# Kernel tuning notes

Hardware: AMD Instinct MI355X
Metric: run time of the kernel (lower is better)

Reference implementation:

```python
import jax, jax.numpy as jnp
import numpy as np

N_NODES = 50000
N_EDGES = 1600000
D_FEAT = 128
EMB = 32
HEADS = 4
SLOPE = 0.2  # PyG GATv2 default negative_slope


def setup_inputs() -> dict:
    key = jax.random.key(0)
    ks = jax.random.split(key, 12)
    H, C = HEADS, EMB
    hid = H * C  # concat output dim = 128

    def glorot(k, shape):
        fan_in, fan_out = shape[0], shape[-1] if len(shape) > 1 else shape[0]
        lim = jnp.sqrt(6.0 / (fan_in + fan_out)).astype(jnp.float32)
        return jax.random.uniform(k, shape, jnp.float32, -lim, lim)

    x = jax.random.normal(ks[0], (N_NODES, D_FEAT), jnp.float32)
    edge_index = jax.random.randint(ks[1], (2, N_EDGES), 0, N_NODES, jnp.int32).astype(jnp.int64)

    return {
        "x": x,
        "edge_index": edge_index,
        # layer 1: in D_FEAT -> H*C (separate source/target lins, share_weights=False)
        "W1_l": glorot(ks[2], (D_FEAT, hid)),
        "W1_r": glorot(ks[3], (D_FEAT, hid)),
        "att1": glorot(ks[4], (H, C)),
        "b1": jnp.zeros((hid,), jnp.float32),
        # layer 2: in H*C -> H*C
        "W2_l": glorot(ks[5], (hid, hid)),
        "W2_r": glorot(ks[6], (hid, hid)),
        "att2": glorot(ks[7], (H, C)),
        "b2": jnp.zeros((hid,), jnp.float32),
    }


def _gatv2_layer(x, src, dst, W_l, W_r, att, bias, n_nodes):
    H, C = att.shape
    xl = (x @ W_l).reshape(n_nodes, H, C)  # source-side transform
    xr = (x @ W_r).reshape(n_nodes, H, C)  # target-side transform
    # per-edge pre-activation: GATv2 applies LeakyReLU BEFORE the attention dot
    msg = xl[src] + xr[dst]                               # [E, H, C]
    e = jnp.einsum('ehc,hc->eh', jax.nn.leaky_relu(msg, SLOPE), att)  # [E, H]
    # numerically stable segment softmax over incoming edges of each dst node
    m = jax.ops.segment_max(e, dst, num_segments=n_nodes)  # [N, H]
    ex = jnp.exp(e - m[dst])
    denom = jax.ops.segment_sum(ex, dst, num_segments=n_nodes)  # [N, H]
    alpha = ex / (denom[dst] + 1e-16)                     # [E, H]
    out = jax.ops.segment_sum(alpha[:, :, None] * xl[src], dst, num_segments=n_nodes)
    return out.reshape(n_nodes, H * C) + bias


def reference(x, edge_index, W1_l, W1_r, att1, b1, W2_l, W2_r, att2, b2):
    n = x.shape[0]
    # PyG default add_self_loops=True: append (i -> i) for every node
    loop = jnp.arange(n, dtype=edge_index.dtype)
    src = jnp.concatenate([edge_index[0], loop])
    dst = jnp.concatenate([edge_index[1], loop])
    h = jax.nn.relu(_gatv2_layer(x, src, dst, W1_l, W1_r, att1, b1, n))
    h = jax.nn.relu(_gatv2_layer(h, src, dst, W2_l, W2_r, att2, b2, n))
    return h
```

## Files before the change

### kernel.cpp

```cpp
#include <hip/hip_runtime.h>

#define N_NODES 50000
#define N_EDGES 1600000
#define ET (N_EDGES + N_NODES)
#define DF 128
#define SLOPE 0.2f

#define NB 196
#define BCAP 10240
#define P1_CHUNK 4096
#define GEMM_BLOCKS ((N_NODES + 63) / 64)
#define BIN_BLOCKS ((ET + P1_CHUNK - 1) / P1_CHUNK)

typedef __attribute__((ext_vector_type(4))) float floatx4;
typedef __attribute__((ext_vector_type(8))) _Float16 half8;
typedef __attribute__((ext_vector_type(2))) _Float16 half2v;

__global__ __launch_bounds__(256) void wconv4(
    const float* __restrict__ W0, const float* __restrict__ W1,
    const float* __restrict__ W2, const float* __restrict__ W3,
    _Float16* __restrict__ Wh, _Float16* __restrict__ Wl,
    int* __restrict__ g_count)
{
    if (blockIdx.x == 0) g_count[threadIdx.x] = 0;
    int idx = blockIdx.x * 256 + threadIdx.x;
    int m = idx >> 14, rem = idx & 16383;
    const float* W = (m == 0) ? W0 : (m == 1) ? W1 : (m == 2) ? W2 : W3;
    int c = rem >> 7, k = rem & 127;
    float v = W[k * 128 + c];
    _Float16 h = (_Float16)v;
    int slab = k >> 5, q = (k >> 3) & 3, j = k & 7;
    size_t o = (size_t)m * 16384 + (size_t)((slab << 2) + q) * 1024 + (c << 3) + j;
    Wh[o] = h;
    Wl[o] = (_Float16)(v - (float)h);
}

__device__ __forceinline__ half8 load_h8(const float* p) {
    float4 a = *(const float4*)(p);
    float4 b = *(const float4*)(p + 4);
    half8 h;
    h[0] = (_Float16)a.x; h[1] = (_Float16)a.y;
    h[2] = (_Float16)a.z; h[3] = (_Float16)a.w;
    h[4] = (_Float16)b.x; h[5] = (_Float16)b.y;
    h[6] = (_Float16)b.z; h[7] = (_Float16)b.w;
    return h;
}
__device__ __forceinline__ half8 load_h8(const _Float16* p) {
    return *(const half8*)p;
}

template<typename T>
__device__ __forceinline__ void gemm_body(
    int bid, const T* __restrict__ X,
    const _Float16* __restrict__ WhL, const _Float16* __restrict__ WlL,
    const _Float16* __restrict__ WhR, const _Float16* __restrict__ WlR,
    _Float16* __restrict__ outL, _Float16* __restrict__ outR, int M, char* smem_)
{
    _Float16* xs  = (_Float16*)smem_;
    _Float16* whL = xs + 64 * 40;
    _Float16* wlL = whL + 4096;
    _Float16* whR = wlL + 4096;
    _Float16* wlR = whR + 4096;

    const int t = threadIdx.x;
    const int row0 = bid * 64;
    const int lane = t & 63, wv = t >> 6;
    const int lm = lane & 15, quad = lane >> 4;
    const int m0 = wv * 16;

    floatx4 accL[8], accR[8];
#pragma unroll
    for (int i = 0; i < 8; i++) { accL[i] = (floatx4)0.f; accR[i] = (floatx4)0.f; }

    const int sr = t >> 2;
    const int sc = (t & 3) * 8;

    for (int kb = 0; kb < 128; kb += 32) {
        const int slab = kb >> 5;
        int xrow = row0 + sr; if (xrow >= M) xrow = M - 1;
        half8 xv = load_h8(X + (size_t)xrow * DF + kb + sc);
        *(half8*)&xs[sr * 40 + sc] = xv;

        {
            const size_t sbase = (size_t)slab * 4096;
            const _Float16* gsrc[4] = { WhL + sbase, WlL + sbase,
                                        WhR + sbase, WlR + sbase };
            _Float16* ldst[4] = { whL, wlL, whR, wlR };
#pragma unroll
            for (int b = 0; b < 4; b++) {
#pragma unroll
                for (int i = 0; i < 2; i++) {
                    const int chunk = wv * 2 + i;
                    const _Float16* src = gsrc[b] + chunk * 512 + lane * 8;
                    __builtin_amdgcn_global_load_lds(
                        (const __attribute__((address_space(1))) void*)src,
                        (__attribute__((address_space(3))) void*)(ldst[b] + chunk * 512),
                        16, 0, 0);
                }
            }
        }
        __syncthreads();

        half8 af = *(const half8*)&xs[(m0 + lm) * 40 + quad * 8];
#pragma unroll
        for (int nt = 0; nt < 8; nt++) {
            const int bofs = quad * 1024 + (nt * 16 + lm) * 8;
            half8 bh = *(const half8*)&whL[bofs];
            half8 bl = *(const half8*)&wlL[bofs];
            accL[nt] = __builtin_amdgcn_mfma_f32_16x16x32_f16(af, bh, accL[nt], 0, 0, 0);
            accL[nt] = __builtin_amdgcn_mfma_f32_16x16x32_f16(af, bl, accL[nt], 0, 0, 0);
            half8 ch = *(const half8*)&whR[bofs];
            half8 cl = *(const half8*)&wlR[bofs];
            accR[nt] = __builtin_amdgcn_mfma_f32_16x16x32_f16(af, ch, accR[nt], 0, 0, 0);
            accR[nt] = __builtin_amdgcn_mfma_f32_16x16x32_f16(af, cl, accR[nt], 0, 0, 0);
        }
        __syncthreads();
    }

#pragma unroll
    for (int nt = 0; nt < 8; nt++) {
        int col = (nt >> 2) * 64 + (nt & 3) * 16 + lm;
#pragma unroll
        for (int r = 0; r < 4; r++) {
            int gr = row0 + m0 + quad * 4 + r;
            if (gr < M) {
                size_t o = (size_t)gr * DF + col;
                outL[o] = (_Float16)accL[nt][r];
                outR[o] = (_Float16)accR[nt][r];
            }
        }
    }
}

__device__ __forceinline__ void bin_body(
    int bid, const int* __restrict__ ei,
    int* __restrict__ g_count, int* __restrict__ bucket_mem, char* smem_)
{
    int* cnt  = (int*)smem_;
    int* base = cnt + NB;
    int* cnt2 = base + NB;
    const int tid = threadIdx.x;

    for (int i = tid; i < NB; i += 256) { cnt[i] = 0; cnt2[i] = 0; }
    __syncthreads();

    const int e0 = bid * P1_CHUNK;
    int srcv[16], dstv[16];
#pragma unroll
    for (int i = 0; i < 16; i++) {
        int eid = e0 + i * 256 + tid;
        int s = 0, d = -1;
        if (eid < ET) {
            if (eid < N_EDGES) { s = ei[eid]; d = ei[N_EDGES + eid]; }
            else               { s = d = eid - N_EDGES; }
        }
        srcv[i] = s; dstv[i] = d;
        if (d >= 0) atomicAdd(&cnt[d >> 8], 1);
    }
    __syncthreads();
    for (int i = tid; i < NB; i += 256)
        base[i] = (cnt[i] > 0) ? atomicAdd(&g_count[i], cnt[i]) : 0;
    __syncthreads();
#pragma unroll
    for (int i = 0; i < 16; i++) {
        int d = dstv[i];
        if (d >= 0) {
            int b = d >> 8;
            int r = atomicAdd(&cnt2[b], 1);
            int slot = base[b] + r;
            if (slot < BCAP)
                bucket_mem[(size_t)b * BCAP + slot] =
                    (srcv[i] & 0xFFFF) | ((d & 255) << 16);
        }
    }
}

__global__ __launch_bounds__(256) void gemm_bin(
    const float* __restrict__ X,
    const _Float16* __restrict__ Wh, const _Float16* __restrict__ Wl,
    _Float16* __restrict__ outL, _Float16* __restrict__ outR,
    const int* __restrict__ ei,
    int* __restrict__ g_count, int* __restrict__ bucket_mem)
{
    __shared__ char smem[37888];
    if (blockIdx.x < GEMM_BLOCKS)
        gemm_body<float>(blockIdx.x, X, Wh, Wl, Wh + 16384, Wl + 16384,
                         outL, outR, N_NODES, smem);
    else
        bin_body(blockIdx.x - GEMM_BLOCKS, ei, g_count, bucket_mem, smem);
}

__global__ __launch_bounds__(256) void gemm_f16(
    const _Float16* __restrict__ X,
    const _Float16* __restrict__ Wh, const _Float16* __restrict__ Wl,
    _Float16* __restrict__ outL, _Float16* __restrict__ outR)
{
    __shared__ char smem[37888];
    gemm_body<_Float16>(blockIdx.x, X, Wh, Wl, Wh + 16384, Wl + 16384,
                        outL, outR, N_NODES, smem);
}

__global__ __launch_bounds__(1024) void csr_pass(const int* __restrict__ g_count,
                                                 const int* __restrict__ bucket_mem,
                                                 int* __restrict__ row_ptr,
                                                 unsigned short* __restrict__ csr_src)
{
    __shared__ int sh_edges[BCAP];
    __shared__ int hist[256], offs[256], excl[256], cnt2[256];
    __shared__ int gsc[256];
    const int b = blockIdx.x, tid = threadIdx.x;

    if (tid < 256) gsc[tid] = (tid < NB) ? g_count[tid] : 0;
    __syncthreads();
    for (int d = 1; d < 256; d <<= 1) {
        int x = 0;
        if (tid < 256 && tid >= d) x = gsc[tid - d];
        __syncthreads();
        if (tid < 256) gsc[tid] += x;
        __syncthreads();
    }
    const int base_csr = (b > 0) ? gsc[b - 1] : 0;

    int m = g_count[b]; if (m > BCAP) m = BCAP;
    if (tid < 256) { hist[tid] = 0; cnt2[tid] = 0; }
    __syncthreads();
    const int* bm = bucket_mem + (size_t)b * BCAP;
    for (int i = tid; i < m; i += 1024) {
        int p = bm[i];
        sh_edges[i] = p;
        atomicAdd(&hist[(p >> 16) & 255], 1);
    }
    __syncthreads();
    if (tid < 256) offs[tid] = hist[tid];
    __syncthreads();
    for (int d = 1; d < 256; d <<= 1) {
        int x = 0;
        if (tid < 256 && tid >= d) x = offs[tid - d];
        __syncthreads();
        if (tid < 256) offs[tid] += x;
        __syncthreads();
    }
    if (tid < 256) {
        excl[tid] = offs[tid] - hist[tid];
        int node = (b << 8) + tid;
        if (node < N_NODES) row_ptr[node] = base_csr + excl[tid];
    }
    if (b == 0 && tid == 0) row_ptr[N_NODES] = ET;
    __syncthreads();
    for (int i = tid; i < m; i += 1024) {
        int p = sh_edges[i];
        int dl = (p >> 16) & 255;
        int r = atomicAdd(&cnt2[dl], 1);
        csr_src[base_csr + excl[dl] + r] = (unsigned short)(p & 0xFFFF);
    }
}

template<typename TOut>
__global__ __launch_bounds__(256) void fused_agg(
    const _Float16* __restrict__ XL, const _Float16* __restrict__ XR,
    const int* __restrict__ row_ptr, const unsigned short* __restrict__ csr_src,
    const float* __restrict__ att, const float* __restrict__ bias,
    TOut* __restrict__ out)
{
    const int t = threadIdx.x;
    const int wave = t >> 6, l = t & 63;
    const int g = l >> 4, gl = l & 15;
    const int n = blockIdx.x * 4 + wave;
    if (n >= N_NODES) return;
    const int beg = row_ptr[n], end = row_ptr[n + 1];
    const int deg = end - beg;
    const int dlim = (deg < 128) ? deg : 128;

    const int liA = beg + l, liB = liA + 64;
    unsigned sa = (liA < end) ? (unsigned)csr_src[liA] : 0u;
    unsigned sb = (liB < end) ? (unsigned)csr_src[liB] : 0u;
    const unsigned s32 = sa | (sb << 16);

    const int c0 = gl * 8;
    half8 xrh = *(const half8*)(XR + (size_t)n * DF + c0);
    float4 at0 = *(const float4*)(att + c0);
    float4 at1 = *(const float4*)(att + c0 + 4);
    half2v a01 = { (_Float16)at0.x, (_Float16)at0.y };
    half2v a23 = { (_Float16)at0.z, (_Float16)at0.w };
    half2v a45 = { (_Float16)at1.x, (_Float16)at1.y };
    half2v a67 = { (_Float16)at1.z, (_Float16)at1.w };
    const half8 slp = { (_Float16)SLOPE, (_Float16)SLOPE, (_Float16)SLOPE, (_Float16)SLOPE,
                        (_Float16)SLOPE, (_Float16)SLOPE, (_Float16)SLOPE, (_Float16)SLOPE };

    float a0 = 0.f, a1 = 0.f, a2 = 0.f, a3 = 0.f;
    float a4 = 0.f, a5 = 0.f, a6 = 0.f, a7 = 0.f, den = 0.f;

#define SRC(POS)                                                               \
    ({ int _p = (POS);                                                         \
       unsigned _v = (unsigned)__shfl((int)s32, _p & 63);                      \
       (int)(((_p & 64) ? (_v >> 16) : _v) & 0xFFFFu); })
#define LDROW(S) (*(const half8*)(XL + ((size_t)(unsigned)(S) << 7) + c0))

#define EDGE_STEP(HV, EOK)                                                     \
    {                                                                          \
        const bool _ok = (EOK);                                                \
        half8 _msg = HV + xrh;                                                 \
        half8 _lk  = __builtin_elementwise_max(_msg, _msg * slp);              \
        half2v _m01 = { _lk[0], _lk[1] };                                      \
        half2v _m23 = { _lk[2], _lk[3] };                                      \
        half2v _m45 = { _lk[4], _lk[5] };                                      \
        half2v _m67 = { _lk[6], _lk[7] };                                      \
        float _sc = __builtin_amdgcn_fdot2(_m01, a01, 0.f, false);             \
        _sc = __builtin_amdgcn_fdot2(_m23, a23, _sc, false);                   \
        _sc = __builtin_amdgcn_fdot2(_m45, a45, _sc, false);                   \
        _sc = __builtin_amdgcn_fdot2(_m67, a67, _sc, false);                   \
        _sc += __shfl_xor(_sc, 1);                                             \
        _sc += __shfl_xor(_sc, 2);                                             \
        float _e = _ok ? __expf(_sc) : 0.f;                                    \
        uint4 _hw; __builtin_memcpy(&_hw, &(HV), 16);                          \
        asm("v_fma_mix_f32 %0, %1, %2, %0 op_sel:[0,0,0] op_sel_hi:[1,0,0]"    \
            : "+v"(a0) : "v"(_hw.x), "v"(_e));                                 \
        asm("v_fma_mix_f32 %0, %1, %2, %0 op_sel:[1,0,0] op_sel_hi:[1,0,0]"    \
            : "+v"(a1) : "v"(_hw.x), "v"(_e));                                 \
        asm("v_fma_mix_f32 %0, %1, %2, %0 op_sel:[0,0,0] op_sel_hi:[1,0,0]"    \
            : "+v"(a2) : "v"(_hw.y), "v"(_e));                                 \
        asm("v_fma_mix_f32 %0, %1, %2, %0 op_sel:[1,0,0] op_sel_hi:[1,0,0]"    \
            : "+v"(a3) : "v"(_hw.y), "v"(_e));                                 \
        asm("v_fma_mix_f32 %0, %1, %2, %0 op_sel:[0,0,0] op_sel_hi:[1,0,0]"    \
            : "+v"(a4) : "v"(_hw.z), "v"(_e));                                 \
        asm("v_fma_mix_f32 %0, %1, %2, %0 op_sel:[1,0,0] op_sel_hi:[1,0,0]"    \
            : "+v"(a5) : "v"(_hw.z), "v"(_e));                                 \
        asm("v_fma_mix_f32 %0, %1, %2, %0 op_sel:[0,0,0] op_sel_hi:[1,0,0]"    \
            : "+v"(a6) : "v"(_hw.w), "v"(_e));                                 \
        asm("v_fma_mix_f32 %0, %1, %2, %0 op_sel:[1,0,0] op_sel_hi:[1,0,0]"    \
            : "+v"(a7) : "v"(_hw.w), "v"(_e));                                 \
        den += _e;                                                             \
    }

    half8 X0 = LDROW(SRC(g));
    half8 X1 = LDROW(SRC(4 + g));
    half8 Y0 = LDROW(SRC(8 + g));
    half8 Y1 = LDROW(SRC(12 + g));

    int p = 0;
    for (;;) {
        EDGE_STEP(X0, (p + g < dlim))
        EDGE_STEP(X1, (p + 4 + g < dlim))
        X0 = LDROW(SRC(p + 16 + g));
        X1 = LDROW(SRC(p + 20 + g));
        p += 8;
        if (p >= dlim) break;
        EDGE_STEP(Y0, (p + g < dlim))
        EDGE_STEP(Y1, (p + 4 + g < dlim))
        Y0 = LDROW(SRC(p + 16 + g));
        Y1 = LDROW(SRC(p + 20 + g));
        p += 8;
        if (p >= dlim) break;
    }

    for (int q = 128; q < deg; q += 4) {
        int ei_ = beg + q + g;
        int s = (ei_ < end) ? (int)csr_src[ei_] : 0;
        half8 hvt = LDROW(s);
        EDGE_STEP(hvt, (q + g < deg))
    }
#undef EDGE_STEP
#undef SRC
#undef LDROW

#define CMB(x) x += __shfl_xor(x, 16); x += __shfl_xor(x, 32);
    CMB(a0) CMB(a1) CMB(a2) CMB(a3) CMB(a4) CMB(a5) CMB(a6) CMB(a7) CMB(den)
#undef CMB

    if (g == 0) {
        float inv = 1.f / (den + 1e-16f);
        float4 b0 = *(const float4*)(bias + c0);
        float4 b1 = *(const float4*)(bias + c0 + 4);
        float o[8];
        o[0] = fmaxf(a0 * inv + b0.x, 0.f);
        o[1] = fmaxf(a1 * inv + b0.y, 0.f);
        o[2] = fmaxf(a2 * inv + b0.z, 0.f);
        o[3] = fmaxf(a3 * inv + b0.w, 0.f);
        o[4] = fmaxf(a4 * inv + b1.x, 0.f);
        o[5] = fmaxf(a5 * inv + b1.y, 0.f);
        o[6] = fmaxf(a6 * inv + b1.z, 0.f);
        o[7] = fmaxf(a7 * inv + b1.w, 0.f);
        TOut* op = out + (size_t)n * DF + c0;
        if constexpr (sizeof(TOut) == 2) {
            half8 hv;
#pragma unroll
            for (int i = 0; i < 8; i++) hv[i] = (_Float16)o[i];
            *(half8*)op = hv;
        } else {
            *(float4*)(op)     = make_float4(o[0], o[1], o[2], o[3]);
            *(float4*)(op + 4) = make_float4(o[4], o[5], o[6], o[7]);
        }
    }
}

extern "C" void kernel_launch(void* const* d_in, const int* in_sizes, int n_in,
                              void* d_out, int out_size, void* d_ws, size_t ws_size,
                              hipStream_t stream)
{
    (void)in_sizes; (void)n_in; (void)out_size; (void)ws_size;

    const float* x    = (const float*)d_in[0];
    const int*   ei   = (const int*)d_in[1];
    const float* W1l  = (const float*)d_in[2];
    const float* W1r  = (const float*)d_in[3];
    const float* att1 = (const float*)d_in[4];
    const float* b1   = (const float*)d_in[5];
    const float* W2l  = (const float*)d_in[6];
    const float* W2r  = (const float*)d_in[7];
    const float* att2 = (const float*)d_in[8];
    const float* b2   = (const float*)d_in[9];
    float* out = (float*)d_out;

    char* ws = (char*)d_ws;
    size_t off = 0;
    const size_t NF = (size_t)N_NODES * DF * sizeof(float);
    _Float16* A = (_Float16*)(ws + off); off += NF / 2;
    _Float16* B = (_Float16*)(ws + off); off += NF / 2;
    _Float16* C = (_Float16*)(ws + off); off += NF / 2;
    int* bucket_mem  = (int*)(ws + off); off += (size_t)NB * BCAP * sizeof(int);
    int* g_count     = (int*)(ws + off); off += 256 * sizeof(int);
    int* row_ptr     = (int*)(ws + off); off += (size_t)(N_NODES + 1) * sizeof(int);
    unsigned short* csr_src = (unsigned short*)(ws + off);
    off += ((size_t)ET * sizeof(unsigned short) + 255) & ~(size_t)255;
    _Float16* Wh = (_Float16*)(ws + off); off += 4 * 16384 * sizeof(_Float16);
    _Float16* Wl = (_Float16*)(ws + off); off += 4 * 16384 * sizeof(_Float16);

    wconv4<<<256, 256, 0, stream>>>(W1l, W1r, W2l, W2r, Wh, Wl, g_count);

    gemm_bin<<<GEMM_BLOCKS + BIN_BLOCKS, 256, 0, stream>>>(
        x, Wh, Wl, A, B, ei, g_count, bucket_mem);
    csr_pass<<<NB, 1024, 0, stream>>>(g_count, bucket_mem, row_ptr, csr_src);
    fused_agg<_Float16><<<(N_NODES + 3) / 4, 256, 0, stream>>>(
        A, B, row_ptr, csr_src, att1, b1, C);

    gemm_f16<<<GEMM_BLOCKS, 256, 0, stream>>>(C, Wh + 2 * 16384, Wl + 2 * 16384, A, B);
    fused_agg<float><<<(N_NODES + 3) / 4, 256, 0, stream>>>(
        A, B, row_ptr, csr_src, att2, b2, out);
}
```

Baseline: 264.3 us.

## Regroup prep kernels: fuse weight conversion with binning, CSR build with GEMM

Edge binning moves out of the GEMM launch and into a new launch alongside weight conversion. The CSR build then runs as extra blocks beside the first-layer GEMM, which removes the standalone 1024-thread csr_pass launch. Buckets shrink from 256 to 128 destination nodes (391 buckets, capacity 6144) so each CSR block fits in 256 threads and shares the GEMM's shared-memory size. The g_count reset becomes a memset. The cost is one more launch (the memset), and bucket overflow is now silently dropped at a smaller per-bucket capacity.

```diff
diff --git a/kernel.cpp b/kernel.cpp
--- a/kernel.cpp
+++ b/kernel.cpp
@@ -6,24 +6,24 @@
 #define DF 128
 #define SLOPE 0.2f
 
-#define NB 196
-#define BCAP 10240
+#define NB2 391
+#define CAP2 6144
 #define P1_CHUNK 4096
 #define GEMM_BLOCKS ((N_NODES + 63) / 64)
 #define BIN_BLOCKS ((ET + P1_CHUNK - 1) / P1_CHUNK)
+#define WCONV_BLOCKS 256
 
 typedef __attribute__((ext_vector_type(4))) float floatx4;
 typedef __attribute__((ext_vector_type(8))) _Float16 half8;
 typedef __attribute__((ext_vector_type(2))) _Float16 half2v;
 
-__global__ __launch_bounds__(256) void wconv4(
+__device__ __forceinline__ void wconv_body(
+    int bid,
     const float* __restrict__ W0, const float* __restrict__ W1,
     const float* __restrict__ W2, const float* __restrict__ W3,
-    _Float16* __restrict__ Wh, _Float16* __restrict__ Wl,
-    int* __restrict__ g_count)
-{
-    if (blockIdx.x == 0) g_count[threadIdx.x] = 0;
-    int idx = blockIdx.x * 256 + threadIdx.x;
+    _Float16* __restrict__ Wh, _Float16* __restrict__ Wl)
+{
+    int idx = bid * 256 + threadIdx.x;
     int m = idx >> 14, rem = idx & 16383;
     const float* W = (m == 0) ? W0 : (m == 1) ? W1 : (m == 2) ? W2 : W3;
     int c = rem >> 7, k = rem & 127;
@@ -33,6 +33,63 @@
     size_t o = (size_t)m * 16384 + (size_t)((slab << 2) + q) * 1024 + (c << 3) + j;
     Wh[o] = h;
     Wl[o] = (_Float16)(v - (float)h);
+}
+
+__device__ __forceinline__ void bin_body(
+    int bid, const int* __restrict__ ei,
+    int* __restrict__ g_count, int* __restrict__ bucket_mem, char* smem_)
+{
+    int* cnt  = (int*)smem_;
+    int* base = cnt + NB2;
+    int* cnt2 = base + NB2;
+    const int tid = threadIdx.x;
+
+    for (int i = tid; i < NB2; i += 256) { cnt[i] = 0; cnt2[i] = 0; }
+    __syncthreads();
+
+    const int e0 = bid * P1_CHUNK;
+    int srcv[16], dstv[16];
+#pragma unroll
+    for (int i = 0; i < 16; i++) {
+        int eid = e0 + i * 256 + tid;
+        int s = 0, d = -1;
+        if (eid < ET) {
+            if (eid < N_EDGES) { s = ei[eid]; d = ei[N_EDGES + eid]; }
+            else               { s = d = eid - N_EDGES; }
+        }
+        srcv[i] = s; dstv[i] = d;
+        if (d >= 0) atomicAdd(&cnt[d >> 7], 1);
+    }
+    __syncthreads();
+    for (int i = tid; i < NB2; i += 256)
+        base[i] = (cnt[i] > 0) ? atomicAdd(&g_count[i], cnt[i]) : 0;
+    __syncthreads();
+#pragma unroll
+    for (int i = 0; i < 16; i++) {
+        int d = dstv[i];
+        if (d >= 0) {
+            int b = d >> 7;
+            int r = atomicAdd(&cnt2[b], 1);
+            int slot = base[b] + r;
+            if (slot < CAP2)
+                bucket_mem[(size_t)b * CAP2 + slot] =
+                    (srcv[i] & 0xFFFF) | ((d & 127) << 16);
+        }
+    }
+}
+
+__global__ __launch_bounds__(256) void prep_bin(
+    const float* __restrict__ W0, const float* __restrict__ W1,
+    const float* __restrict__ W2, const float* __restrict__ W3,
+    _Float16* __restrict__ Wh, _Float16* __restrict__ Wl,
+    const int* __restrict__ ei,
+    int* __restrict__ g_count, int* __restrict__ bucket_mem)
+{
+    __shared__ char smem[4704];
+    if (blockIdx.x < WCONV_BLOCKS)
+        wconv_body(blockIdx.x, W0, W1, W2, W3, Wh, Wl);
+    else
+        bin_body(blockIdx.x - WCONV_BLOCKS, ei, g_count, bucket_mem, smem);
 }
 
 __device__ __forceinline__ half8 load_h8(const float* p) {
@@ -132,62 +189,78 @@
     }
 }
 
-__device__ __forceinline__ void bin_body(
-    int bid, const int* __restrict__ ei,
-    int* __restrict__ g_count, int* __restrict__ bucket_mem, char* smem_)
-{
-    int* cnt  = (int*)smem_;
-    int* base = cnt + NB;
-    int* cnt2 = base + NB;
+__device__ __forceinline__ void csr_body(
+    int b, const int* __restrict__ g_count, const int* __restrict__ bucket_mem,
+    int* __restrict__ row_ptr, unsigned short* __restrict__ csr_src, char* smem_)
+{
+    int* sh_edges = (int*)smem_;
+    int* hist = sh_edges + 6144;
+    int* excl = hist + 128;
+    int* cnt2 = excl + 128;
+    int* sA   = cnt2 + 128;
+    int* sB   = sA + 512;
     const int tid = threadIdx.x;
 
-    for (int i = tid; i < NB; i += 256) { cnt[i] = 0; cnt2[i] = 0; }
-    __syncthreads();
-
-    const int e0 = bid * P1_CHUNK;
-    int srcv[16], dstv[16];
-#pragma unroll
-    for (int i = 0; i < 16; i++) {
-        int eid = e0 + i * 256 + tid;
-        int s = 0, d = -1;
-        if (eid < ET) {
-            if (eid < N_EDGES) { s = ei[eid]; d = ei[N_EDGES + eid]; }
-            else               { s = d = eid - N_EDGES; }
-        }
-        srcv[i] = s; dstv[i] = d;
-        if (d >= 0) atomicAdd(&cnt[d >> 8], 1);
-    }
-    __syncthreads();
-    for (int i = tid; i < NB; i += 256)
-        base[i] = (cnt[i] > 0) ? atomicAdd(&g_count[i], cnt[i]) : 0;
-    __syncthreads();
-#pragma unroll
-    for (int i = 0; i < 16; i++) {
-        int d = dstv[i];
-        if (d >= 0) {
-            int b = d >> 8;
-            int r = atomicAdd(&cnt2[b], 1);
-            int slot = base[b] + r;
-            if (slot < BCAP)
-                bucket_mem[(size_t)b * BCAP + slot] =
-                    (srcv[i] & 0xFFFF) | ((d & 255) << 16);
-        }
-    }
-}
-
-__global__ __launch_bounds__(256) void gemm_bin(
+    sA[tid]       = (tid < NB2)       ? g_count[tid]       : 0;
+    sA[tid + 256] = (tid + 256 < NB2) ? g_count[tid + 256] : 0;
+    __syncthreads();
+    int* in = sA; int* outp = sB;
+    for (int d = 1; d < 512; d <<= 1) {
+        for (int i = tid; i < 512; i += 256)
+            outp[i] = in[i] + ((i >= d) ? in[i - d] : 0);
+        __syncthreads();
+        int* tmp = in; in = outp; outp = tmp;
+    }
+    const int base_csr = (b > 0) ? in[b - 1] : 0;
+
+    int m = g_count[b]; if (m > CAP2) m = CAP2;
+    if (tid < 128) { hist[tid] = 0; cnt2[tid] = 0; }
+    __syncthreads();
+    const int* bm = bucket_mem + (size_t)b * CAP2;
+    for (int i = tid; i < m; i += 256) {
+        int p = bm[i];
+        sh_edges[i] = p;
+        atomicAdd(&hist[(p >> 16) & 127], 1);
+    }
+    __syncthreads();
+    if (tid < 128) sA[tid] = hist[tid];
+    __syncthreads();
+    for (int d = 1; d < 128; d <<= 1) {
+        int x = 0;
+        if (tid < 128 && tid >= d) x = sA[tid - d];
+        __syncthreads();
+        if (tid < 128) sA[tid] += x;
+        __syncthreads();
+    }
+    if (tid < 128) {
+        excl[tid] = sA[tid] - hist[tid];
+        int node = (b << 7) + tid;
+        if (node < N_NODES) row_ptr[node] = base_csr + excl[tid];
+    }
+    if (b == 0 && tid == 0) row_ptr[N_NODES] = ET;
+    __syncthreads();
+    for (int i = tid; i < m; i += 256) {
+        int p = sh_edges[i];
+        int dl = (p >> 16) & 127;
+        int r = atomicAdd(&cnt2[dl], 1);
+        csr_src[base_csr + excl[dl] + r] = (unsigned short)(p & 0xFFFF);
+    }
+}
+
+__global__ __launch_bounds__(256) void gemm_csr(
     const float* __restrict__ X,
     const _Float16* __restrict__ Wh, const _Float16* __restrict__ Wl,
     _Float16* __restrict__ outL, _Float16* __restrict__ outR,
-    const int* __restrict__ ei,
-    int* __restrict__ g_count, int* __restrict__ bucket_mem)
+    const int* __restrict__ g_count, const int* __restrict__ bucket_mem,
+    int* __restrict__ row_ptr, unsigned short* __restrict__ csr_src)
 {
     __shared__ char smem[37888];
     if (blockIdx.x < GEMM_BLOCKS)
         gemm_body<float>(blockIdx.x, X, Wh, Wl, Wh + 16384, Wl + 16384,
                          outL, outR, N_NODES, smem);
     else
-        bin_body(blockIdx.x - GEMM_BLOCKS, ei, g_count, bucket_mem, smem);
+        csr_body(blockIdx.x - GEMM_BLOCKS, g_count, bucket_mem,
+                 row_ptr, csr_src, smem);
 }
 
 __global__ __launch_bounds__(256) void gemm_f16(
@@ -198,61 +271,6 @@
     __shared__ char smem[37888];
     gemm_body<_Float16>(blockIdx.x, X, Wh, Wl, Wh + 16384, Wl + 16384,
                         outL, outR, N_NODES, smem);
-}
-
-__global__ __launch_bounds__(1024) void csr_pass(const int* __restrict__ g_count,
-                                                 const int* __restrict__ bucket_mem,
-                                                 int* __restrict__ row_ptr,
-                                                 unsigned short* __restrict__ csr_src)
-{
-    __shared__ int sh_edges[BCAP];
-    __shared__ int hist[256], offs[256], excl[256], cnt2[256];
-    __shared__ int gsc[256];
-    const int b = blockIdx.x, tid = threadIdx.x;
-
-    if (tid < 256) gsc[tid] = (tid < NB) ? g_count[tid] : 0;
-    __syncthreads();
-    for (int d = 1; d < 256; d <<= 1) {
-        int x = 0;
-        if (tid < 256 && tid >= d) x = gsc[tid - d];
-        __syncthreads();
-        if (tid < 256) gsc[tid] += x;
-        __syncthreads();
-    }
-    const int base_csr = (b > 0) ? gsc[b - 1] : 0;
-
-    int m = g_count[b]; if (m > BCAP) m = BCAP;
-    if (tid < 256) { hist[tid] = 0; cnt2[tid] = 0; }
-    __syncthreads();
-    const int* bm = bucket_mem + (size_t)b * BCAP;
-    for (int i = tid; i < m; i += 1024) {
-        int p = bm[i];
-        sh_edges[i] = p;
-        atomicAdd(&hist[(p >> 16) & 255], 1);
-    }
-    __syncthreads();
-    if (tid < 256) offs[tid] = hist[tid];
-    __syncthreads();
-    for (int d = 1; d < 256; d <<= 1) {
-        int x = 0;
-        if (tid < 256 && tid >= d) x = offs[tid - d];
-        __syncthreads();
-        if (tid < 256) offs[tid] += x;
-        __syncthreads();
-    }
-    if (tid < 256) {
-        excl[tid] = offs[tid] - hist[tid];
-        int node = (b << 8) + tid;
-        if (node < N_NODES) row_ptr[node] = base_csr + excl[tid];
-    }
-    if (b == 0 && tid == 0) row_ptr[N_NODES] = ET;
-    __syncthreads();
-    for (int i = tid; i < m; i += 1024) {
-        int p = sh_edges[i];
-        int dl = (p >> 16) & 255;
-        int r = atomicAdd(&cnt2[dl], 1);
-        csr_src[base_csr + excl[dl] + r] = (unsigned short)(p & 0xFFFF);
-    }
 }
 
 template<typename TOut>
@@ -417,19 +435,22 @@
     _Float16* A = (_Float16*)(ws + off); off += NF / 2;
     _Float16* B = (_Float16*)(ws + off); off += NF / 2;
     _Float16* C = (_Float16*)(ws + off); off += NF / 2;
-    int* bucket_mem  = (int*)(ws + off); off += (size_t)NB * BCAP * sizeof(int);
-    int* g_count     = (int*)(ws + off); off += 256 * sizeof(int);
+    int* bucket_mem  = (int*)(ws + off); off += (size_t)NB2 * CAP2 * sizeof(int);
+    int* g_count     = (int*)(ws + off); off += 512 * sizeof(int);
     int* row_ptr     = (int*)(ws + off); off += (size_t)(N_NODES + 1) * sizeof(int);
     unsigned short* csr_src = (unsigned short*)(ws + off);
     off += ((size_t)ET * sizeof(unsigned short) + 255) & ~(size_t)255;
     _Float16* Wh = (_Float16*)(ws + off); off += 4 * 16384 * sizeof(_Float16);
     _Float16* Wl = (_Float16*)(ws + off); off += 4 * 16384 * sizeof(_Float16);
 
-    wconv4<<<256, 256, 0, stream>>>(W1l, W1r, W2l, W2r, Wh, Wl, g_count);
-
-    gemm_bin<<<GEMM_BLOCKS + BIN_BLOCKS, 256, 0, stream>>>(
-        x, Wh, Wl, A, B, ei, g_count, bucket_mem);
-    csr_pass<<<NB, 1024, 0, stream>>>(g_count, bucket_mem, row_ptr, csr_src);
+    hipMemsetAsync(g_count, 0, 512 * sizeof(int), stream);
+
+    prep_bin<<<WCONV_BLOCKS + BIN_BLOCKS, 256, 0, stream>>>(
+        W1l, W1r, W2l, W2r, Wh, Wl, ei, g_count, bucket_mem);
+
+    gemm_csr<<<GEMM_BLOCKS + NB2, 256, 0, stream>>>(
+        x, Wh, Wl, A, B, g_count, bucket_mem, row_ptr, csr_src);
+
     fused_agg<_Float16><<<(N_NODES + 3) / 4, 256, 0, stream>>>(
         A, B, row_ptr, csr_src, att1, b1, C);
 
```

Result: no change. 267.8 us (+1.3%).
